# Optimization experiments

Measured on AMD Instinct MI355X. Metric: run time of the kernel, lower is better.

The kernel has to match this reference:

```python
import jax, jax.numpy as jnp
import numpy as np


def setup_inputs() -> dict:
    key = jax.random.key(0)
    ks = jax.random.split(key, 8)
    E = 2_000_000          # num facts (edges)
    B, M = 8, 2000         # batch, max_local_entity -> B*M = 16000 entity slots
    R, D = 2000, 128       # num relations, hidden size (in_features == out_features)
    return {
        "local_entity": jax.random.randint(ks[0], (B, M), 0, M),
        "batch_heads": jax.random.randint(ks[1], (E,), 0, B * M),
        "batch_tails": jax.random.randint(ks[2], (E,), 0, B * M),
        "batch_rels": jax.random.randint(ks[3], (E,), 0, R),
        "val_one": jax.random.uniform(ks[4], (E,), dtype=jnp.float32),
        "rel_features": jax.random.normal(ks[5], (R, D), dtype=jnp.float32),
        "W": jax.random.normal(ks[6], (D, D), dtype=jnp.float32) * 0.05,
        "b": jax.random.normal(ks[7], (D,), dtype=jnp.float32) * 0.05,
    }


def reference(local_entity, batch_heads, batch_tails, batch_rels, val_one,
              rel_features, W, b):
    B, M = local_entity.shape
    num_ent = B * M
    # gather relation features per fact, linear transform (nn.Linear: x @ W.T + b)
    fact_rel = rel_features[batch_rels]            # [E, D]
    fact_val = fact_rel @ W.T + b                  # [E, D]
    # sparse COO mm == weighted scatter-add of fact_val into entity slots
    weighted = fact_val * val_one[:, None]         # [E, D]
    tail_agg = jax.ops.segment_sum(weighted, batch_tails, num_segments=num_ent)
    head_agg = jax.ops.segment_sum(weighted, batch_heads, num_segments=num_ent)
    f2e_emb = jax.nn.relu(tail_agg + head_agg)     # [B*M, D]
    return f2e_emb.reshape(B, M, -1)
```

## Files before the change

### kernel.cpp

```cpp
#include <hip/hip_runtime.h>
#include <hip/hip_bf16.h>
#include <cstdint>

typedef _Float16 half2v __attribute__((ext_vector_type(2)));

#define EPB   16
#define MAXNB 1024
#define FPB   4096
#define FPT   4
#define SORTCAP 4608
#define CPT   9


__device__ __forceinline__ float pay_val(unsigned p) {
    return (float)__builtin_bit_cast(_Float16, (unsigned short)(p & 0xFFFFu));
}

__global__ void rwb_row_kernel(const float* __restrict__ rel, const float* __restrict__ W,
                               const float* __restrict__ b, _Float16* __restrict__ rwb,
                               int R, int* __restrict__ gcnt, float* __restrict__ out,
                               int NB, int NUMENT) {
    const int k = blockIdx.x;
    const int n = threadIdx.x;
    const int gtid = k * 128 + n;
    const int gstr = gridDim.x * 128;
    for (int i = gtid; i < NB; i += gstr) gcnt[i] = 0;
    const int n4 = NUMENT * 32;
    const float4 z = {0.f, 0.f, 0.f, 0.f};
    for (int i = gtid; i < n4; i += gstr)
        reinterpret_cast<float4*>(out)[i] = z;

    __shared__ float relk[128];
    relk[n] = rel[(size_t)k * 128 + n];
    __syncthreads();
    const float4* w4 = reinterpret_cast<const float4*>(W + (size_t)n * 128);
    const float4* r4 = reinterpret_cast<const float4*>(relk);
    float acc = 0.f;
#pragma unroll
    for (int i = 0; i < 32; ++i) {
        float4 a = r4[i], w = w4[i];
        acc += a.x * w.x + a.y * w.y + a.z * w.z + a.w * w.w;
    }
    rwb[(size_t)k * 128 + n] = (_Float16)(acc + b[n]);
}

__device__ __noinline__ void spill_add(float* __restrict__ out, const _Float16* __restrict__ rwb,
                                       int v, unsigned pay) {
    const int r = (int)((pay >> 16) & 0xFFFu);
    const float val = pay_val(pay);
    float* o = out + (size_t)v * 128;
    const _Float16* rw = rwb + (size_t)r * 128;
    for (int n = 0; n < 128; ++n) unsafeAtomicAdd(o + n, val * (float)rw[n]);
}

__global__ __launch_bounds__(1024) void bin_kernel(
    const int* __restrict__ heads, const int* __restrict__ tails,
    const int* __restrict__ rels, const float* __restrict__ val,
    int* __restrict__ gcnt, unsigned* __restrict__ slots,
    const _Float16* __restrict__ rwb, float* __restrict__ out,
    int E, int NB, int CAPB) {
    __shared__ int cnt[MAXNB];
    __shared__ int gbase[MAXNB];
    const int t = threadIdx.x;
    for (int k = t; k < NB; k += 1024) cnt[k] = 0;
    __syncthreads();

    const int i0 = blockIdx.x * FPB + t * FPT;
    unsigned payT[FPT], payH[FPT], prT[FPT], prH[FPT];
#pragma unroll
    for (int u = 0; u < FPT; ++u) { prT[u] = 0xFFFFFFFFu; prH[u] = 0xFFFFFFFFu; }

    int tl[FPT], hd[FPT], rr[FPT];
    float vv[FPT];
    int nval = 0;
    if (i0 + FPT <= E) {
        const int4 T  = *reinterpret_cast<const int4*>(tails + i0);
        const int4 H  = *reinterpret_cast<const int4*>(heads + i0);
        const int4 Rv = *reinterpret_cast<const int4*>(rels + i0);
        const float4 Vv = *reinterpret_cast<const float4*>(val + i0);
        tl[0] = T.x;  tl[1] = T.y;  tl[2] = T.z;  tl[3] = T.w;
        hd[0] = H.x;  hd[1] = H.y;  hd[2] = H.z;  hd[3] = H.w;
        rr[0] = Rv.x; rr[1] = Rv.y; rr[2] = Rv.z; rr[3] = Rv.w;
        vv[0] = Vv.x; vv[1] = Vv.y; vv[2] = Vv.z; vv[3] = Vv.w;
        nval = FPT;
    } else {
#pragma unroll
        for (int u = 0; u < FPT; ++u) {
            const int i = i0 + u;
            if (i < E) {
                tl[u] = tails[i]; hd[u] = heads[i];
                rr[u] = rels[i];  vv[u] = val[i];
                nval = u + 1;
            }
        }
    }
#pragma unroll
    for (int u = 0; u < FPT; ++u) {
        if (u < nval) {
            const unsigned hv =
                (unsigned)__builtin_bit_cast(unsigned short, (_Float16)vv[u]);
            const int bt = tl[u] >> 4, bh = hd[u] >> 4;
            payT[u] = ((unsigned)(tl[u] & 15) << 28) | ((unsigned)rr[u] << 16) | hv;
            payH[u] = ((unsigned)(hd[u] & 15) << 28) | ((unsigned)rr[u] << 16) | hv;
            const int rt = atomicAdd(&cnt[bt], 1);
            const int rh = atomicAdd(&cnt[bh], 1);
            prT[u] = ((unsigned)bt << 16) | (unsigned)rt;
            prH[u] = ((unsigned)bh << 16) | (unsigned)rh;
        }
    }
    __syncthreads();
    for (int k = t; k < NB; k += 1024) {
        const int c = cnt[k];
        gbase[k] = c ? atomicAdd(&gcnt[k], c) : 0;
    }
    __syncthreads();
#pragma unroll
    for (int u = 0; u < FPT; ++u) {
        if (prT[u] != 0xFFFFFFFFu) {
            {
                const int b1 = (int)(prT[u] >> 16);
                const int pos = gbase[b1] + (int)(prT[u] & 0xFFFFu);
                if (pos < CAPB) slots[(size_t)b1 * CAPB + pos] = payT[u];
                else spill_add(out, rwb, (b1 << 4) | (int)(payT[u] >> 28), payT[u]);
            }
            {
                const int b1 = (int)(prH[u] >> 16);
                const int pos = gbase[b1] + (int)(prH[u] & 0xFFFFu);
                if (pos < CAPB) slots[(size_t)b1 * CAPB + pos] = payH[u];
                else spill_add(out, rwb, (b1 << 4) | (int)(payH[u] >> 28), payH[u]);
            }
        }
    }
}

__global__ __launch_bounds__(512) void gather_kernel(
    const unsigned* __restrict__ slots, const int* __restrict__ gcnt,
    const _Float16* __restrict__ rwb, float* __restrict__ out,
    int NUMENT, int CAPB) {
    __shared__ unsigned se[SORTCAP];
    __shared__ int cnt[EPB], basep[EPB];
    const int t = threadIdx.x;
    const int b = blockIdx.x;
    if (t < EPB) cnt[t] = 0;
    __syncthreads();

    int deg = gcnt[b];
    if (deg > CAPB) deg = CAPB;
    const unsigned* sl = slots + (size_t)b * CAPB;

    unsigned e[CPT];
    int rk[CPT];
#pragma unroll
    for (int u = 0; u < CPT; ++u) {
        const int k = t + u * 512;
        rk[u] = -1;
        if (k < deg) {
            e[u] = sl[k];
            rk[u] = atomicAdd(&cnt[(int)(e[u] >> 28)], 1);
        }
    }
    __syncthreads();
    if (t == 0) {
        int s = 0;
#pragma unroll
        for (int i = 0; i < EPB; ++i) { basep[i] = s; s += cnt[i]; }
    }
    __syncthreads();
#pragma unroll
    for (int u = 0; u < CPT; ++u)
        if (rk[u] >= 0) se[basep[(int)(e[u] >> 28)] + rk[u]] = e[u];
    __syncthreads();

    const int wv = t >> 6, lane = t & 63;
    const int loff = lane * 2;
#pragma unroll
    for (int ei = 0; ei < 2; ++ei) {
        const int le = wv * 2 + ei;
        const int vent = b * EPB + le;
        const int s0 = basep[le], c = cnt[le];
        float a0 = 0.f, a1 = 0.f;
        int j = 0;
        for (; j + 8 <= c; j += 8) {
            uint2 qp[4];
#pragma unroll
            for (int u = 0; u < 4; ++u)
                qp[u] = *reinterpret_cast<const uint2*>(&se[s0 + j + 2 * u]);
            unsigned qs[8];
#pragma unroll
            for (int u = 0; u < 4; ++u) {
                qs[2 * u]     = __builtin_amdgcn_readfirstlane(qp[u].x);
                qs[2 * u + 1] = __builtin_amdgcn_readfirstlane(qp[u].y);
            }
            unsigned rw[8];
#pragma unroll
            for (int u = 0; u < 8; ++u) {
                const _Float16* rowp = rwb + (size_t)((qs[u] >> 16) & 0xFFFu) * 128;
                rw[u] = *reinterpret_cast<const unsigned*>(rowp + loff);
            }
#pragma unroll
            for (int u = 0; u < 8; ++u) {
                asm("v_fma_mix_f32 %[d], %[s0], %[s1], %[d] op_sel:[0,0,0] op_sel_hi:[1,1,0]"
                    : [d]"+v"(a0) : [s0]"s"(qs[u]), [s1]"v"(rw[u]));
                asm("v_fma_mix_f32 %[d], %[s0], %[s1], %[d] op_sel:[0,1,0] op_sel_hi:[1,1,0]"
                    : [d]"+v"(a1) : [s0]"s"(qs[u]), [s1]"v"(rw[u]));
            }
        }
        for (; j < c; ++j) {
            const unsigned q = se[s0 + j];
            const unsigned qs = __builtin_amdgcn_readfirstlane(q);
            const _Float16* rowp = rwb + (size_t)((qs >> 16) & 0xFFFu) * 128;
            const unsigned rwv = *reinterpret_cast<const unsigned*>(rowp + loff);
            asm("v_fma_mix_f32 %[d], %[s0], %[s1], %[d] op_sel:[0,0,0] op_sel_hi:[1,1,0]"
                : [d]"+v"(a0) : [s0]"s"(qs), [s1]"v"(rwv));
            asm("v_fma_mix_f32 %[d], %[s0], %[s1], %[d] op_sel:[0,1,0] op_sel_hi:[1,1,0]"
                : [d]"+v"(a1) : [s0]"s"(qs), [s1]"v"(rwv));
        }
        if (vent < NUMENT) {
            float* op = out + (size_t)vent * 128 + loff;
            float2 sp = *reinterpret_cast<const float2*>(op);
            float2 o;
            o.x = fmaxf(a0 + sp.x, 0.f);
            o.y = fmaxf(a1 + sp.y, 0.f);
            *reinterpret_cast<float2*>(op) = o;
        }
    }
}

__global__ void rwb_f32_kernel(const float* __restrict__ rel, const float* __restrict__ W,
                               const float* __restrict__ b, float* __restrict__ rwb, int R) {
    const int k = blockIdx.x;
    const int n = threadIdx.x;
    __shared__ float relk[128];
    relk[n] = rel[(size_t)k * 128 + n];
    __syncthreads();
    const float4* w4 = reinterpret_cast<const float4*>(W + (size_t)n * 128);
    const float4* r4 = reinterpret_cast<const float4*>(relk);
    float acc = 0.f;
#pragma unroll
    for (int i = 0; i < 32; ++i) {
        float4 a = r4[i], w = w4[i];
        acc += a.x * w.x + a.y * w.y + a.z * w.z + a.w * w.w;
    }
    rwb[(size_t)k * 128 + n] = acc + b[n];
}

__global__ void scatter_vec_kernel(const int* __restrict__ heads, const int* __restrict__ tails,
                                   const int* __restrict__ rels, const float* __restrict__ val,
                                   const float* __restrict__ rwb, float* __restrict__ out,
                                   long long nitems) {
    const long long i = (long long)blockIdx.x * blockDim.x + threadIdx.x;
    if (i >= nitems) return;
    const int e = (int)(i >> 5);
    const int c = (int)(i & 31) * 4;
    const float v = val[e];
    float4 rw = *reinterpret_cast<const float4*>(rwb + (size_t)rels[e] * 128 + c);
    float* pt = out + (size_t)tails[e] * 128 + c;
    float* ph = out + (size_t)heads[e] * 128 + c;
    unsafeAtomicAdd(pt + 0, v * rw.x); unsafeAtomicAdd(pt + 1, v * rw.y);
    unsafeAtomicAdd(pt + 2, v * rw.z); unsafeAtomicAdd(pt + 3, v * rw.w);
    unsafeAtomicAdd(ph + 0, v * rw.x); unsafeAtomicAdd(ph + 1, v * rw.y);
    unsafeAtomicAdd(ph + 2, v * rw.z); unsafeAtomicAdd(ph + 3, v * rw.w);
}

__global__ void relu_kernel(float* __restrict__ out, int n4) {
    const int i = blockIdx.x * blockDim.x + threadIdx.x;
    if (i >= n4) return;
    float4* p = reinterpret_cast<float4*>(out) + i;
    float4 v = *p;
    v.x = fmaxf(v.x, 0.f); v.y = fmaxf(v.y, 0.f);
    v.z = fmaxf(v.z, 0.f); v.w = fmaxf(v.w, 0.f);
    *p = v;
}

extern "C" void kernel_launch(void* const* d_in, const int* in_sizes, int n_in,
                              void* d_out, int out_size, void* d_ws, size_t ws_size,
                              hipStream_t stream) {
    const int* heads = (const int*)d_in[1];
    const int* tails = (const int*)d_in[2];
    const int* rels  = (const int*)d_in[3];
    const float* val  = (const float*)d_in[4];
    const float* relf = (const float*)d_in[5];
    const float* W    = (const float*)d_in[6];
    const float* b    = (const float*)d_in[7];
    float* out = (float*)d_out;

    const int NUMENT = in_sizes[0];
    const int E      = in_sizes[1];
    const int D      = in_sizes[7];
    const int R      = in_sizes[5] / D;

    const int NB = (NUMENT + EPB - 1) / EPB;
    const long long mean = (2LL * E * EPB) / (NUMENT > 0 ? NUMENT : 1);
    int CAPB = (int)(mean + mean / 16 + 256);

    const size_t rwb_bytes = (size_t)R * D * sizeof(_Float16);
    const size_t off_gcnt  = (rwb_bytes + 255) & ~(size_t)255;
    const size_t gcnt_b    = (size_t)NB * sizeof(int);
    const size_t off_slots = (off_gcnt + gcnt_b + 255) & ~(size_t)255;
    const size_t slots_b   = (size_t)NB * CAPB * sizeof(unsigned);

    if (NB <= MAXNB && R < 4096 && CAPB <= SORTCAP &&
        ws_size >= off_slots + slots_b) {
        _Float16* rwb   = (_Float16*)d_ws;
        int* gcnt       = (int*)((char*)d_ws + off_gcnt);
        unsigned* slots = (unsigned*)((char*)d_ws + off_slots);

        rwb_row_kernel<<<R, 128, 0, stream>>>(relf, W, b, rwb, R, gcnt, out, NB, NUMENT);
        bin_kernel<<<(E + FPB - 1) / FPB, 1024, 0, stream>>>(
            heads, tails, rels, val, gcnt, slots, rwb, out, E, NB, CAPB);
        gather_kernel<<<NB, 512, 0, stream>>>(slots, gcnt, rwb, out, NUMENT, CAPB);
    } else {
        float* rwb = (float*)d_ws;
        hipMemsetAsync(out, 0, (size_t)out_size * sizeof(float), stream);
        rwb_f32_kernel<<<R, 128, 0, stream>>>(relf, W, b, rwb, R);
        const long long items = (long long)E * 32;
        scatter_vec_kernel<<<(unsigned)((items + 255) / 256), 256, 0, stream>>>(
            heads, tails, rels, val, rwb, out, items);
        relu_kernel<<<(out_size / 4 + 255) / 256, 256, 0, stream>>>(out, out_size / 4);
    }
}
```

Baseline: 188.4 us.

## Fuse binning, relation transform and gather into one persistent kernel

Replaces the three launches (rwb transform with output zeroing, binning, gather) with a single persistent kernel of 512 blocks. Binning and the relation-weight transform run first, then a spin-wait global barrier, then the gather phase. Capacity overflow no longer does per-element atomics into a pre-zeroed output. It goes to a small global overflow list that each gather wave scans, so the full output memset is dropped and the gather writes relu(acc) directly. The design depends on all 512 blocks being co-resident for the barrier, and the overflow scan is linear in the overflow count per entity.

```diff
diff --git a/kernel.cpp b/kernel.cpp
--- a/kernel.cpp
+++ b/kernel.cpp
@@ -4,224 +4,255 @@
 
 typedef _Float16 half2v __attribute__((ext_vector_type(2)));
 
-#define EPB   16
-#define MAXNB 1024
-#define FPB   4096
-#define FPT   4
+#define EPB    16
+#define MAXNB  1024
+#define FPT    8
+#define FPB    4096
 #define SORTCAP 4608
-#define CPT   9
-
-
-__device__ __forceinline__ float pay_val(unsigned p) {
-    return (float)__builtin_bit_cast(_Float16, (unsigned short)(p & 0xFFFFu));
-}
-
-__global__ void rwb_row_kernel(const float* __restrict__ rel, const float* __restrict__ W,
-                               const float* __restrict__ b, _Float16* __restrict__ rwb,
-                               int R, int* __restrict__ gcnt, float* __restrict__ out,
-                               int NB, int NUMENT) {
-    const int k = blockIdx.x;
-    const int n = threadIdx.x;
-    const int gtid = k * 128 + n;
-    const int gstr = gridDim.x * 128;
-    for (int i = gtid; i < NB; i += gstr) gcnt[i] = 0;
-    const int n4 = NUMENT * 32;
-    const float4 z = {0.f, 0.f, 0.f, 0.f};
-    for (int i = gtid; i < n4; i += gstr)
-        reinterpret_cast<float4*>(out)[i] = z;
-
-    __shared__ float relk[128];
-    relk[n] = rel[(size_t)k * 128 + n];
+#define CPT    9
+#define GRID   512
+#define OVFCAP 65536
+
+
+__device__ __forceinline__ void grid_barrier(int* bar, int nblk) {
     __syncthreads();
-    const float4* w4 = reinterpret_cast<const float4*>(W + (size_t)n * 128);
-    const float4* r4 = reinterpret_cast<const float4*>(relk);
-    float acc = 0.f;
-#pragma unroll
-    for (int i = 0; i < 32; ++i) {
-        float4 a = r4[i], w = w4[i];
-        acc += a.x * w.x + a.y * w.y + a.z * w.z + a.w * w.w;
-    }
-    rwb[(size_t)k * 128 + n] = (_Float16)(acc + b[n]);
-}
-
-__device__ __noinline__ void spill_add(float* __restrict__ out, const _Float16* __restrict__ rwb,
-                                       int v, unsigned pay) {
-    const int r = (int)((pay >> 16) & 0xFFFu);
-    const float val = pay_val(pay);
-    float* o = out + (size_t)v * 128;
-    const _Float16* rw = rwb + (size_t)r * 128;
-    for (int n = 0; n < 128; ++n) unsafeAtomicAdd(o + n, val * (float)rw[n]);
-}
-
-__global__ __launch_bounds__(1024) void bin_kernel(
+    if (threadIdx.x == 0) {
+        __threadfence();
+        atomicAdd(bar, 1);
+        long long guard = 0;
+        while (__hip_atomic_load(bar, __ATOMIC_ACQUIRE,
+                                 __HIP_MEMORY_SCOPE_AGENT) < nblk) {
+            __builtin_amdgcn_s_sleep(8);
+            if (++guard > 200000000LL) break;
+        }
+        __threadfence();
+    }
+    __syncthreads();
+}
+
+__global__ __launch_bounds__(512, 4) void fused_kernel(
     const int* __restrict__ heads, const int* __restrict__ tails,
     const int* __restrict__ rels, const float* __restrict__ val,
-    int* __restrict__ gcnt, unsigned* __restrict__ slots,
-    const _Float16* __restrict__ rwb, float* __restrict__ out,
-    int E, int NB, int CAPB) {
-    __shared__ int cnt[MAXNB];
-    __shared__ int gbase[MAXNB];
+    const float* __restrict__ relf, const float* __restrict__ W,
+    const float* __restrict__ bias,
+    _Float16* __restrict__ rwb, int* __restrict__ gcnt,
+    int* __restrict__ bar, int* __restrict__ ovfcnt, uint2* __restrict__ ovf,
+    unsigned* __restrict__ slots, float* __restrict__ out,
+    int E, int R, int NB, int CAPB, int NUMENT)
+{
+    __shared__ union {
+        struct { int cnt[MAXNB]; int gbase[MAXNB]; } bin;
+        struct { unsigned se[SORTCAP]; int cnt[EPB]; int basep[EPB]; } gat;
+    } sh;
     const int t = threadIdx.x;
-    for (int k = t; k < NB; k += 1024) cnt[k] = 0;
-    __syncthreads();
-
-    const int i0 = blockIdx.x * FPB + t * FPT;
-    unsigned payT[FPT], payH[FPT], prT[FPT], prH[FPT];
-#pragma unroll
-    for (int u = 0; u < FPT; ++u) { prT[u] = 0xFFFFFFFFu; prH[u] = 0xFFFFFFFFu; }
-
-    int tl[FPT], hd[FPT], rr[FPT];
-    float vv[FPT];
-    int nval = 0;
-    if (i0 + FPT <= E) {
-        const int4 T  = *reinterpret_cast<const int4*>(tails + i0);
-        const int4 H  = *reinterpret_cast<const int4*>(heads + i0);
-        const int4 Rv = *reinterpret_cast<const int4*>(rels + i0);
-        const float4 Vv = *reinterpret_cast<const float4*>(val + i0);
-        tl[0] = T.x;  tl[1] = T.y;  tl[2] = T.z;  tl[3] = T.w;
-        hd[0] = H.x;  hd[1] = H.y;  hd[2] = H.z;  hd[3] = H.w;
-        rr[0] = Rv.x; rr[1] = Rv.y; rr[2] = Rv.z; rr[3] = Rv.w;
-        vv[0] = Vv.x; vv[1] = Vv.y; vv[2] = Vv.z; vv[3] = Vv.w;
-        nval = FPT;
-    } else {
+
+    for (long long cb = blockIdx.x; cb * FPB < (long long)E; cb += GRID) {
+        for (int k = t; k < NB; k += 512) sh.bin.cnt[k] = 0;
+        __syncthreads();
+
+        const int i0 = (int)(cb * FPB) + t * FPT;
+        unsigned payT[FPT], payH[FPT], prT[FPT], prH[FPT];
+#pragma unroll
+        for (int u = 0; u < FPT; ++u) { prT[u] = 0xFFFFFFFFu; prH[u] = 0xFFFFFFFFu; }
+
+        int tl[FPT], hd[FPT], rr[FPT];
+        float vv[FPT];
+        int nval = 0;
+        if (i0 + FPT <= E) {
+            *reinterpret_cast<int4*>(&tl[0]) = *reinterpret_cast<const int4*>(tails + i0);
+            *reinterpret_cast<int4*>(&tl[4]) = *reinterpret_cast<const int4*>(tails + i0 + 4);
+            *reinterpret_cast<int4*>(&hd[0]) = *reinterpret_cast<const int4*>(heads + i0);
+            *reinterpret_cast<int4*>(&hd[4]) = *reinterpret_cast<const int4*>(heads + i0 + 4);
+            *reinterpret_cast<int4*>(&rr[0]) = *reinterpret_cast<const int4*>(rels + i0);
+            *reinterpret_cast<int4*>(&rr[4]) = *reinterpret_cast<const int4*>(rels + i0 + 4);
+            *reinterpret_cast<float4*>(&vv[0]) = *reinterpret_cast<const float4*>(val + i0);
+            *reinterpret_cast<float4*>(&vv[4]) = *reinterpret_cast<const float4*>(val + i0 + 4);
+            nval = FPT;
+        } else {
+#pragma unroll
+            for (int u = 0; u < FPT; ++u) {
+                const int i = i0 + u;
+                if (i < E) {
+                    tl[u] = tails[i]; hd[u] = heads[i];
+                    rr[u] = rels[i];  vv[u] = val[i];
+                    nval = u + 1;
+                }
+            }
+        }
 #pragma unroll
         for (int u = 0; u < FPT; ++u) {
-            const int i = i0 + u;
-            if (i < E) {
-                tl[u] = tails[i]; hd[u] = heads[i];
-                rr[u] = rels[i];  vv[u] = val[i];
-                nval = u + 1;
-            }
-        }
-    }
-#pragma unroll
-    for (int u = 0; u < FPT; ++u) {
-        if (u < nval) {
-            const unsigned hv =
-                (unsigned)__builtin_bit_cast(unsigned short, (_Float16)vv[u]);
-            const int bt = tl[u] >> 4, bh = hd[u] >> 4;
-            payT[u] = ((unsigned)(tl[u] & 15) << 28) | ((unsigned)rr[u] << 16) | hv;
-            payH[u] = ((unsigned)(hd[u] & 15) << 28) | ((unsigned)rr[u] << 16) | hv;
-            const int rt = atomicAdd(&cnt[bt], 1);
-            const int rh = atomicAdd(&cnt[bh], 1);
-            prT[u] = ((unsigned)bt << 16) | (unsigned)rt;
-            prH[u] = ((unsigned)bh << 16) | (unsigned)rh;
-        }
-    }
-    __syncthreads();
-    for (int k = t; k < NB; k += 1024) {
-        const int c = cnt[k];
-        gbase[k] = c ? atomicAdd(&gcnt[k], c) : 0;
-    }
-    __syncthreads();
-#pragma unroll
-    for (int u = 0; u < FPT; ++u) {
-        if (prT[u] != 0xFFFFFFFFu) {
-            {
-                const int b1 = (int)(prT[u] >> 16);
-                const int pos = gbase[b1] + (int)(prT[u] & 0xFFFFu);
-                if (pos < CAPB) slots[(size_t)b1 * CAPB + pos] = payT[u];
-                else spill_add(out, rwb, (b1 << 4) | (int)(payT[u] >> 28), payT[u]);
-            }
-            {
-                const int b1 = (int)(prH[u] >> 16);
-                const int pos = gbase[b1] + (int)(prH[u] & 0xFFFFu);
-                if (pos < CAPB) slots[(size_t)b1 * CAPB + pos] = payH[u];
-                else spill_add(out, rwb, (b1 << 4) | (int)(payH[u] >> 28), payH[u]);
-            }
-        }
-    }
-}
-
-__global__ __launch_bounds__(512) void gather_kernel(
-    const unsigned* __restrict__ slots, const int* __restrict__ gcnt,
-    const _Float16* __restrict__ rwb, float* __restrict__ out,
-    int NUMENT, int CAPB) {
-    __shared__ unsigned se[SORTCAP];
-    __shared__ int cnt[EPB], basep[EPB];
-    const int t = threadIdx.x;
-    const int b = blockIdx.x;
-    if (t < EPB) cnt[t] = 0;
-    __syncthreads();
-
-    int deg = gcnt[b];
-    if (deg > CAPB) deg = CAPB;
-    const unsigned* sl = slots + (size_t)b * CAPB;
-
-    unsigned e[CPT];
-    int rk[CPT];
-#pragma unroll
-    for (int u = 0; u < CPT; ++u) {
-        const int k = t + u * 512;
-        rk[u] = -1;
-        if (k < deg) {
-            e[u] = sl[k];
-            rk[u] = atomicAdd(&cnt[(int)(e[u] >> 28)], 1);
-        }
-    }
-    __syncthreads();
-    if (t == 0) {
-        int s = 0;
-#pragma unroll
-        for (int i = 0; i < EPB; ++i) { basep[i] = s; s += cnt[i]; }
-    }
-    __syncthreads();
-#pragma unroll
-    for (int u = 0; u < CPT; ++u)
-        if (rk[u] >= 0) se[basep[(int)(e[u] >> 28)] + rk[u]] = e[u];
-    __syncthreads();
-
+            if (u < nval) {
+                const unsigned hv =
+                    (unsigned)__builtin_bit_cast(unsigned short, (_Float16)vv[u]);
+                const int bt = tl[u] >> 4, bh = hd[u] >> 4;
+                payT[u] = ((unsigned)(tl[u] & 15) << 28) | ((unsigned)rr[u] << 16) | hv;
+                payH[u] = ((unsigned)(hd[u] & 15) << 28) | ((unsigned)rr[u] << 16) | hv;
+                const int rt = atomicAdd(&sh.bin.cnt[bt], 1);
+                const int rh = atomicAdd(&sh.bin.cnt[bh], 1);
+                prT[u] = ((unsigned)bt << 16) | (unsigned)rt;
+                prH[u] = ((unsigned)bh << 16) | (unsigned)rh;
+            }
+        }
+        __syncthreads();
+        for (int k = t; k < NB; k += 512) {
+            const int c = sh.bin.cnt[k];
+            sh.bin.gbase[k] = c ? atomicAdd(&gcnt[k], c) : 0;
+        }
+        __syncthreads();
+#pragma unroll
+        for (int u = 0; u < FPT; ++u) {
+            if (prT[u] != 0xFFFFFFFFu) {
+                {
+                    const int b1 = (int)(prT[u] >> 16);
+                    const int pos = sh.bin.gbase[b1] + (int)(prT[u] & 0xFFFFu);
+                    if (pos < CAPB) slots[(size_t)b1 * CAPB + pos] = payT[u];
+                    else {
+                        const int op = atomicAdd(ovfcnt, 1);
+                        if (op < OVFCAP) {
+                            uint2 o;
+                            o.x = ((unsigned)b1 << 16) | ((payT[u] >> 28) << 12) |
+                                  ((payT[u] >> 16) & 0xFFFu);
+                            o.y = __float_as_uint(vv[u]);
+                            ovf[op] = o;
+                        }
+                    }
+                }
+                {
+                    const int b1 = (int)(prH[u] >> 16);
+                    const int pos = sh.bin.gbase[b1] + (int)(prH[u] & 0xFFFFu);
+                    if (pos < CAPB) slots[(size_t)b1 * CAPB + pos] = payH[u];
+                    else {
+                        const int op = atomicAdd(ovfcnt, 1);
+                        if (op < OVFCAP) {
+                            uint2 o;
+                            o.x = ((unsigned)b1 << 16) | ((payH[u] >> 28) << 12) |
+                                  ((payH[u] >> 16) & 0xFFFu);
+                            o.y = __float_as_uint(vv[u]);
+                            ovf[op] = o;
+                        }
+                    }
+                }
+            }
+        }
+        __syncthreads();
+    }
+
+    for (int r4 = blockIdx.x; r4 * 4 < R; r4 += GRID) {
+        const int row = r4 * 4 + (t >> 7);
+        const int col = t & 127;
+        if (row < R) {
+            const float4* rp = reinterpret_cast<const float4*>(relf + (size_t)row * 128);
+            const float4* wp = reinterpret_cast<const float4*>(W + (size_t)col * 128);
+            float acc = 0.f;
+#pragma unroll
+            for (int i = 0; i < 32; ++i) {
+                float4 a = rp[i], w = wp[i];
+                acc += a.x * w.x + a.y * w.y + a.z * w.z + a.w * w.w;
+            }
+            rwb[(size_t)row * 128 + col] = (_Float16)(acc + bias[col]);
+        }
+    }
+
+    grid_barrier(bar, GRID);
+
+    const int novf = min(__hip_atomic_load(ovfcnt, __ATOMIC_RELAXED,
+                                           __HIP_MEMORY_SCOPE_AGENT), OVFCAP);
     const int wv = t >> 6, lane = t & 63;
     const int loff = lane * 2;
-#pragma unroll
-    for (int ei = 0; ei < 2; ++ei) {
-        const int le = wv * 2 + ei;
-        const int vent = b * EPB + le;
-        const int s0 = basep[le], c = cnt[le];
-        float a0 = 0.f, a1 = 0.f;
-        int j = 0;
-        for (; j + 8 <= c; j += 8) {
-            uint2 qp[4];
-#pragma unroll
-            for (int u = 0; u < 4; ++u)
-                qp[u] = *reinterpret_cast<const uint2*>(&se[s0 + j + 2 * u]);
-            unsigned qs[8];
-#pragma unroll
-            for (int u = 0; u < 4; ++u) {
-                qs[2 * u]     = __builtin_amdgcn_readfirstlane(qp[u].x);
-                qs[2 * u + 1] = __builtin_amdgcn_readfirstlane(qp[u].y);
-            }
-            unsigned rw[8];
-#pragma unroll
-            for (int u = 0; u < 8; ++u) {
-                const _Float16* rowp = rwb + (size_t)((qs[u] >> 16) & 0xFFFu) * 128;
-                rw[u] = *reinterpret_cast<const unsigned*>(rowp + loff);
-            }
-#pragma unroll
-            for (int u = 0; u < 8; ++u) {
+
+    for (int bk = blockIdx.x; bk < NB; bk += GRID) {
+        __syncthreads();
+        if (t < EPB) sh.gat.cnt[t] = 0;
+        __syncthreads();
+
+        int deg = gcnt[bk];
+        if (deg > CAPB) deg = CAPB;
+        const unsigned* sl = slots + (size_t)bk * CAPB;
+
+        unsigned e[CPT];
+        int rk[CPT];
+#pragma unroll
+        for (int u = 0; u < CPT; ++u) {
+            const int k = t + u * 512;
+            rk[u] = -1;
+            if (k < deg) {
+                e[u] = sl[k];
+                rk[u] = atomicAdd(&sh.gat.cnt[(int)(e[u] >> 28)], 1);
+            }
+        }
+        __syncthreads();
+        if (t == 0) {
+            int s = 0;
+#pragma unroll
+            for (int i = 0; i < EPB; ++i) { sh.gat.basep[i] = s; s += sh.gat.cnt[i]; }
+        }
+        __syncthreads();
+#pragma unroll
+        for (int u = 0; u < CPT; ++u)
+            if (rk[u] >= 0) sh.gat.se[sh.gat.basep[(int)(e[u] >> 28)] + rk[u]] = e[u];
+        __syncthreads();
+
+#pragma unroll
+        for (int ei = 0; ei < 2; ++ei) {
+            const int le = wv * 2 + ei;
+            const int vent = bk * EPB + le;
+            const int s0 = sh.gat.basep[le], c = sh.gat.cnt[le];
+            float a0 = 0.f, a1 = 0.f;
+            int j = 0;
+            for (; j + 8 <= c; j += 8) {
+                uint2 qp[4];
+#pragma unroll
+                for (int u = 0; u < 4; ++u)
+                    qp[u] = *reinterpret_cast<const uint2*>(&sh.gat.se[s0 + j + 2 * u]);
+                unsigned qs[8];
+#pragma unroll
+                for (int u = 0; u < 4; ++u) {
+                    qs[2 * u]     = __builtin_amdgcn_readfirstlane(qp[u].x);
+                    qs[2 * u + 1] = __builtin_amdgcn_readfirstlane(qp[u].y);
+                }
+                unsigned rw[8];
+#pragma unroll
+                for (int u = 0; u < 8; ++u) {
+                    const _Float16* rowp = rwb + (size_t)((qs[u] >> 16) & 0xFFFu) * 128;
+                    rw[u] = *reinterpret_cast<const unsigned*>(rowp + loff);
+                }
+#pragma unroll
+                for (int u = 0; u < 8; ++u) {
+                    asm("v_fma_mix_f32 %[d], %[s0], %[s1], %[d] op_sel:[0,0,0] op_sel_hi:[1,1,0]"
+                        : [d]"+v"(a0) : [s0]"s"(qs[u]), [s1]"v"(rw[u]));
+                    asm("v_fma_mix_f32 %[d], %[s0], %[s1], %[d] op_sel:[0,1,0] op_sel_hi:[1,1,0]"
+                        : [d]"+v"(a1) : [s0]"s"(qs[u]), [s1]"v"(rw[u]));
+                }
+            }
+            for (; j < c; ++j) {
+                const unsigned q = sh.gat.se[s0 + j];
+                const unsigned qs = __builtin_amdgcn_readfirstlane(q);
+                const _Float16* rowp = rwb + (size_t)((qs >> 16) & 0xFFFu) * 128;
+                const unsigned rwv = *reinterpret_cast<const unsigned*>(rowp + loff);
                 asm("v_fma_mix_f32 %[d], %[s0], %[s1], %[d] op_sel:[0,0,0] op_sel_hi:[1,1,0]"
-                    : [d]"+v"(a0) : [s0]"s"(qs[u]), [s1]"v"(rw[u]));
+                    : [d]"+v"(a0) : [s0]"s"(qs), [s1]"v"(rwv));
                 asm("v_fma_mix_f32 %[d], %[s0], %[s1], %[d] op_sel:[0,1,0] op_sel_hi:[1,1,0]"
-                    : [d]"+v"(a1) : [s0]"s"(qs[u]), [s1]"v"(rw[u]));
-            }
-        }
-        for (; j < c; ++j) {
-            const unsigned q = se[s0 + j];
-            const unsigned qs = __builtin_amdgcn_readfirstlane(q);
-            const _Float16* rowp = rwb + (size_t)((qs >> 16) & 0xFFFu) * 128;
-            const unsigned rwv = *reinterpret_cast<const unsigned*>(rowp + loff);
-            asm("v_fma_mix_f32 %[d], %[s0], %[s1], %[d] op_sel:[0,0,0] op_sel_hi:[1,1,0]"
-                : [d]"+v"(a0) : [s0]"s"(qs), [s1]"v"(rwv));
-            asm("v_fma_mix_f32 %[d], %[s0], %[s1], %[d] op_sel:[0,1,0] op_sel_hi:[1,1,0]"
-                : [d]"+v"(a1) : [s0]"s"(qs), [s1]"v"(rwv));
-        }
-        if (vent < NUMENT) {
-            float* op = out + (size_t)vent * 128 + loff;
-            float2 sp = *reinterpret_cast<const float2*>(op);
-            float2 o;
-            o.x = fmaxf(a0 + sp.x, 0.f);
-            o.y = fmaxf(a1 + sp.y, 0.f);
-            *reinterpret_cast<float2*>(op) = o;
+                    : [d]"+v"(a1) : [s0]"s"(qs), [s1]"v"(rwv));
+            }
+            for (int k = 0; k < novf; ++k) {
+                const uint2 o = ovf[k];
+                if ((int)(o.x >> 16) == bk && (int)((o.x >> 12) & 15u) == le) {
+                    const int orel = (int)(o.x & 0xFFFu);
+                    const float ov = __uint_as_float(o.y);
+                    const unsigned orw = *reinterpret_cast<const unsigned*>(
+                        rwb + (size_t)orel * 128 + loff);
+                    const half2v oh = __builtin_bit_cast(half2v, orw);
+                    a0 += ov * (float)oh[0];
+                    a1 += ov * (float)oh[1];
+                }
+            }
+            if (vent < NUMENT) {
+                float* op = out + (size_t)vent * 128 + loff;
+                float2 o2;
+                o2.x = fmaxf(a0, 0.f);
+                o2.y = fmaxf(a1, 0.f);
+                *reinterpret_cast<float2*>(op) = o2;
+            }
         }
     }
 }
@@ -294,21 +325,27 @@
     int CAPB = (int)(mean + mean / 16 + 256);
 
     const size_t rwb_bytes = (size_t)R * D * sizeof(_Float16);
-    const size_t off_gcnt  = (rwb_bytes + 255) & ~(size_t)255;
-    const size_t gcnt_b    = (size_t)NB * sizeof(int);
-    const size_t off_slots = (off_gcnt + gcnt_b + 255) & ~(size_t)255;
+    const size_t off_ctrl  = (rwb_bytes + 255) & ~(size_t)255;
+    const size_t ctrl_b    = (size_t)(NB + 2) * sizeof(int);
+    const size_t off_ovf   = (off_ctrl + ctrl_b + 255) & ~(size_t)255;
+    const size_t ovf_b     = (size_t)OVFCAP * sizeof(uint2);
+    const size_t off_slots = (off_ovf + ovf_b + 255) & ~(size_t)255;
     const size_t slots_b   = (size_t)NB * CAPB * sizeof(unsigned);
 
     if (NB <= MAXNB && R < 4096 && CAPB <= SORTCAP &&
         ws_size >= off_slots + slots_b) {
         _Float16* rwb   = (_Float16*)d_ws;
-        int* gcnt       = (int*)((char*)d_ws + off_gcnt);
+        int* gcnt       = (int*)((char*)d_ws + off_ctrl);
+        int* bar        = gcnt + NB;
+        int* ovfcnt     = gcnt + NB + 1;
+        uint2* ovf      = (uint2*)((char*)d_ws + off_ovf);
         unsigned* slots = (unsigned*)((char*)d_ws + off_slots);
 
-        rwb_row_kernel<<<R, 128, 0, stream>>>(relf, W, b, rwb, R, gcnt, out, NB, NUMENT);
-        bin_kernel<<<(E + FPB - 1) / FPB, 1024, 0, stream>>>(
-            heads, tails, rels, val, gcnt, slots, rwb, out, E, NB, CAPB);
-        gather_kernel<<<NB, 512, 0, stream>>>(slots, gcnt, rwb, out, NUMENT, CAPB);
+        hipMemsetAsync(gcnt, 0, ctrl_b, stream);
+        fused_kernel<<<GRID, 512, 0, stream>>>(
+            heads, tails, rels, val, relf, W, b,
+            rwb, gcnt, bar, ovfcnt, ovf, slots, out,
+            E, R, NB, CAPB, NUMENT);
     } else {
         float* rwb = (float*)d_ws;
         hipMemsetAsync(out, 0, (size_t)out_size * sizeof(float), stream);
```

After: 340.4 us. 80.7% more time.

## Fuse rwb projection into bin kernel and replace spill atomics with overflow list

Applied to the files above, without the earlier changes.

Folds the relation-feature linear projection into the tail of the binning kernel and drops the separate zeroing pass over the output. Bucket overflow entries are now appended to a global overflow list, which the gather kernel scans, instead of being atomically added into the output. The gather kernel writes the output directly without a read-modify-write, and a small memset clears the counters. This removes one launch and an 8 MB zero-fill plus read-back. The cost is that every gather block loops over the whole overflow list. The projection is computed inside the binning kernel, yet the binning kernel itself reads no rwb, so gather still sees a complete table.

```diff
diff --git a/kernel.cpp b/kernel.cpp
--- a/kernel.cpp
+++ b/kernel.cpp
@@ -10,55 +10,17 @@
 #define FPT   4
 #define SORTCAP 4608
 #define CPT   9
-
-
-__device__ __forceinline__ float pay_val(unsigned p) {
-    return (float)__builtin_bit_cast(_Float16, (unsigned short)(p & 0xFFFFu));
-}
-
-__global__ void rwb_row_kernel(const float* __restrict__ rel, const float* __restrict__ W,
-                               const float* __restrict__ b, _Float16* __restrict__ rwb,
-                               int R, int* __restrict__ gcnt, float* __restrict__ out,
-                               int NB, int NUMENT) {
-    const int k = blockIdx.x;
-    const int n = threadIdx.x;
-    const int gtid = k * 128 + n;
-    const int gstr = gridDim.x * 128;
-    for (int i = gtid; i < NB; i += gstr) gcnt[i] = 0;
-    const int n4 = NUMENT * 32;
-    const float4 z = {0.f, 0.f, 0.f, 0.f};
-    for (int i = gtid; i < n4; i += gstr)
-        reinterpret_cast<float4*>(out)[i] = z;
-
-    __shared__ float relk[128];
-    relk[n] = rel[(size_t)k * 128 + n];
-    __syncthreads();
-    const float4* w4 = reinterpret_cast<const float4*>(W + (size_t)n * 128);
-    const float4* r4 = reinterpret_cast<const float4*>(relk);
-    float acc = 0.f;
-#pragma unroll
-    for (int i = 0; i < 32; ++i) {
-        float4 a = r4[i], w = w4[i];
-        acc += a.x * w.x + a.y * w.y + a.z * w.z + a.w * w.w;
-    }
-    rwb[(size_t)k * 128 + n] = (_Float16)(acc + b[n]);
-}
-
-__device__ __noinline__ void spill_add(float* __restrict__ out, const _Float16* __restrict__ rwb,
-                                       int v, unsigned pay) {
-    const int r = (int)((pay >> 16) & 0xFFFu);
-    const float val = pay_val(pay);
-    float* o = out + (size_t)v * 128;
-    const _Float16* rw = rwb + (size_t)r * 128;
-    for (int n = 0; n < 128; ++n) unsafeAtomicAdd(o + n, val * (float)rw[n]);
-}
-
-__global__ __launch_bounds__(1024) void bin_kernel(
+#define OVFCAP 65536
+
+
+__global__ __launch_bounds__(1024) void bin_rwb_kernel(
     const int* __restrict__ heads, const int* __restrict__ tails,
     const int* __restrict__ rels, const float* __restrict__ val,
-    int* __restrict__ gcnt, unsigned* __restrict__ slots,
-    const _Float16* __restrict__ rwb, float* __restrict__ out,
-    int E, int NB, int CAPB) {
+    const float* __restrict__ relf, const float* __restrict__ W,
+    const float* __restrict__ bias, _Float16* __restrict__ rwb,
+    int* __restrict__ gcnt, int* __restrict__ ovfcnt, uint2* __restrict__ ovf,
+    unsigned* __restrict__ slots,
+    int E, int R, int NB, int CAPB) {
     __shared__ int cnt[MAXNB];
     __shared__ int gbase[MAXNB];
     const int t = threadIdx.x;
@@ -121,20 +83,56 @@
                 const int b1 = (int)(prT[u] >> 16);
                 const int pos = gbase[b1] + (int)(prT[u] & 0xFFFFu);
                 if (pos < CAPB) slots[(size_t)b1 * CAPB + pos] = payT[u];
-                else spill_add(out, rwb, (b1 << 4) | (int)(payT[u] >> 28), payT[u]);
+                else {
+                    const int op = atomicAdd(ovfcnt, 1);
+                    if (op < OVFCAP) {
+                        uint2 o;
+                        o.x = ((unsigned)b1 << 16) | ((payT[u] >> 28) << 12) |
+                              ((payT[u] >> 16) & 0xFFFu);
+                        o.y = __float_as_uint(vv[u]);
+                        ovf[op] = o;
+                    }
+                }
             }
             {
                 const int b1 = (int)(prH[u] >> 16);
                 const int pos = gbase[b1] + (int)(prH[u] & 0xFFFFu);
                 if (pos < CAPB) slots[(size_t)b1 * CAPB + pos] = payH[u];
-                else spill_add(out, rwb, (b1 << 4) | (int)(payH[u] >> 28), payH[u]);
-            }
+                else {
+                    const int op = atomicAdd(ovfcnt, 1);
+                    if (op < OVFCAP) {
+                        uint2 o;
+                        o.x = ((unsigned)b1 << 16) | ((payH[u] >> 28) << 12) |
+                              ((payH[u] >> 16) & 0xFFFu);
+                        o.y = __float_as_uint(vv[u]);
+                        ovf[op] = o;
+                    }
+                }
+            }
+        }
+    }
+
+    const int rsub = t >> 7;
+    const int col  = t & 127;
+    for (int row0 = blockIdx.x * 8; row0 < R; row0 += gridDim.x * 8) {
+        const int row = row0 + rsub;
+        if (row < R) {
+            const float4* rp = reinterpret_cast<const float4*>(relf + (size_t)row * 128);
+            const float4* wp = reinterpret_cast<const float4*>(W + (size_t)col * 128);
+            float acc = 0.f;
+#pragma unroll
+            for (int i = 0; i < 32; ++i) {
+                float4 a = rp[i], w = wp[i];
+                acc += a.x * w.x + a.y * w.y + a.z * w.z + a.w * w.w;
+            }
+            rwb[(size_t)row * 128 + col] = (_Float16)(acc + bias[col]);
         }
     }
 }
 
 __global__ __launch_bounds__(512) void gather_kernel(
     const unsigned* __restrict__ slots, const int* __restrict__ gcnt,
+    const int* __restrict__ ovfcnt, const uint2* __restrict__ ovf,
     const _Float16* __restrict__ rwb, float* __restrict__ out,
     int NUMENT, int CAPB) {
     __shared__ unsigned se[SORTCAP];
@@ -170,6 +168,8 @@
     for (int u = 0; u < CPT; ++u)
         if (rk[u] >= 0) se[basep[(int)(e[u] >> 28)] + rk[u]] = e[u];
     __syncthreads();
+
+    const int novf = min(*ovfcnt, OVFCAP);
 
     const int wv = t >> 6, lane = t & 63;
     const int loff = lane * 2;
@@ -215,13 +215,24 @@
             asm("v_fma_mix_f32 %[d], %[s0], %[s1], %[d] op_sel:[0,1,0] op_sel_hi:[1,1,0]"
                 : [d]"+v"(a1) : [s0]"s"(qs), [s1]"v"(rwv));
         }
+        for (int k = 0; k < novf; ++k) {
+            const uint2 o = ovf[k];
+            if ((int)(o.x >> 16) == b && (int)((o.x >> 12) & 15u) == le) {
+                const int orel = (int)(o.x & 0xFFFu);
+                const float ov = __uint_as_float(o.y);
+                const unsigned orw = *reinterpret_cast<const unsigned*>(
+                    rwb + (size_t)orel * 128 + loff);
+                const half2v oh = __builtin_bit_cast(half2v, orw);
+                a0 += ov * (float)oh[0];
+                a1 += ov * (float)oh[1];
+            }
+        }
         if (vent < NUMENT) {
             float* op = out + (size_t)vent * 128 + loff;
-            float2 sp = *reinterpret_cast<const float2*>(op);
-            float2 o;
-            o.x = fmaxf(a0 + sp.x, 0.f);
-            o.y = fmaxf(a1 + sp.y, 0.f);
-            *reinterpret_cast<float2*>(op) = o;
+            float2 o2;
+            o2.x = fmaxf(a0, 0.f);
+            o2.y = fmaxf(a1, 0.f);
+            *reinterpret_cast<float2*>(op) = o2;
         }
     }
 }
@@ -294,21 +305,27 @@
     int CAPB = (int)(mean + mean / 16 + 256);
 
     const size_t rwb_bytes = (size_t)R * D * sizeof(_Float16);
-    const size_t off_gcnt  = (rwb_bytes + 255) & ~(size_t)255;
-    const size_t gcnt_b    = (size_t)NB * sizeof(int);
-    const size_t off_slots = (off_gcnt + gcnt_b + 255) & ~(size_t)255;
+    const size_t off_ctrl  = (rwb_bytes + 255) & ~(size_t)255;
+    const size_t ctrl_b    = (size_t)(NB + 1) * sizeof(int);
+    const size_t off_ovf   = (off_ctrl + ctrl_b + 255) & ~(size_t)255;
+    const size_t ovf_b     = (size_t)OVFCAP * sizeof(uint2);
+    const size_t off_slots = (off_ovf + ovf_b + 255) & ~(size_t)255;
     const size_t slots_b   = (size_t)NB * CAPB * sizeof(unsigned);
 
     if (NB <= MAXNB && R < 4096 && CAPB <= SORTCAP &&
         ws_size >= off_slots + slots_b) {
         _Float16* rwb   = (_Float16*)d_ws;
-        int* gcnt       = (int*)((char*)d_ws + off_gcnt);
+        int* gcnt       = (int*)((char*)d_ws + off_ctrl);
+        int* ovfcnt     = gcnt + NB;
+        uint2* ovf      = (uint2*)((char*)d_ws + off_ovf);
         unsigned* slots = (unsigned*)((char*)d_ws + off_slots);
 
-        rwb_row_kernel<<<R, 128, 0, stream>>>(relf, W, b, rwb, R, gcnt, out, NB, NUMENT);
-        bin_kernel<<<(E + FPB - 1) / FPB, 1024, 0, stream>>>(
-            heads, tails, rels, val, gcnt, slots, rwb, out, E, NB, CAPB);
-        gather_kernel<<<NB, 512, 0, stream>>>(slots, gcnt, rwb, out, NUMENT, CAPB);
+        hipMemsetAsync(gcnt, 0, ctrl_b, stream);
+        bin_rwb_kernel<<<(E + FPB - 1) / FPB, 1024, 0, stream>>>(
+            heads, tails, rels, val, relf, W, b, rwb,
+            gcnt, ovfcnt, ovf, slots, E, R, NB, CAPB);
+        gather_kernel<<<NB, 512, 0, stream>>>(
+            slots, gcnt, ovfcnt, ovf, rwb, out, NUMENT, CAPB);
     } else {
         float* rwb = (float*)d_ws;
         hipMemsetAsync(out, 0, (size_t)out_size * sizeof(float), stream);
```

Result: no change. 187.8 us (-0.3%).
